# Performance work log

Hardware: AMD Instinct MI355X
Metric: run time of the kernel (lower is better)

Reference implementation:

```python
import jax, jax.numpy as jnp
import numpy as np

B, L, ENC, DEC, ATT = 128, 196, 2048, 512, 512

def setup_inputs() -> dict:
    key = jax.random.key(0)
    ks = jax.random.split(key, 8)
    s_enc = 1.0 / np.sqrt(ENC)
    s_dec = 1.0 / np.sqrt(DEC)
    s_att = 1.0 / np.sqrt(ATT)
    return {
        "encoder_out": jax.random.normal(ks[0], (B, L, ENC), jnp.float32),
        "decoder_hidden": jax.random.normal(ks[1], (B, DEC), jnp.float32),
        "We": jax.random.uniform(ks[2], (ENC, ATT), jnp.float32, -s_enc, s_enc),
        "be": jax.random.uniform(ks[3], (ATT,), jnp.float32, -s_enc, s_enc),
        "Wd": jax.random.uniform(ks[4], (DEC, ATT), jnp.float32, -s_dec, s_dec),
        "bd": jax.random.uniform(ks[5], (ATT,), jnp.float32, -s_dec, s_dec),
        "wa": jax.random.uniform(ks[6], (ATT,), jnp.float32, -s_att, s_att),
        "ba": jax.random.uniform(ks[7], (), jnp.float32, -s_att, s_att),
    }

def reference(encoder_out, decoder_hidden, We, be, Wd, bd, wa, ba):
    # encoder_out: [B, L, ENC]; decoder_hidden: [B, DEC]
    enc_map = jnp.einsum('ble,ea->bla', encoder_out, We) + be          # [B, L, A]
    dec_map = decoder_hidden @ Wd + bd                                  # [B, A]
    scores = jnp.tanh(enc_map + dec_map[:, None, :]) @ wa + ba         # [B, L]
    alphas = jax.nn.softmax(scores, axis=1)                             # [B, L]
    context = jnp.einsum('bl,ble->be', alphas, encoder_out)             # [B, ENC]
    return (context, alphas)
```

## Files before the change

kernel.cpp:

```cpp
#include <hip/hip_runtime.h>

#define B_   128
#define L_   196
#define ENC_ 2048
#define DEC_ 512
#define ATT_ 512
#define M_   (B_ * L_)

typedef _Float16 f16x8 __attribute__((ext_vector_type(8)));
typedef __fp16   h16x2 __attribute__((ext_vector_type(2)));
typedef float    f32x4 __attribute__((ext_vector_type(4)));

#define FENCE_LDS_BARRIER()                                        \
    do {                                                           \
        asm volatile("s_waitcnt lgkmcnt(0)" ::: "memory");         \
        __builtin_amdgcn_s_barrier();                              \
        __builtin_amdgcn_sched_barrier(0);                         \
    } while (0)

__device__ __forceinline__ void gload16(const _Float16* g, _Float16* l) {
    __builtin_amdgcn_global_load_lds(
        (const __attribute__((address_space(1))) void*)g,
        (__attribute__((address_space(3))) void*)l, 16, 0, 0);
}


__global__ void wets2_kernel(const float* __restrict__ We, _Float16* __restrict__ WeTs) {
    int u = blockIdx.x * 256 + threadIdx.x;
    int col = u & 255;
    int k8  = (u >> 8) & 3;
    int kt  = (u >> 10) & 63;
    int nt  = u >> 16;
    int n  = nt * 256 + col;
    int k0 = kt * 32 + k8 * 8;
    f16x8 h;
#pragma unroll
    for (int j = 0; j < 8; ++j) h[j] = (_Float16)We[(k0 + j) * ATT_ + n];
    *reinterpret_cast<f16x8*>(WeTs + (size_t)u * 8) = h;
}

__global__ void decmap_kernel(const float* __restrict__ dh, const float* __restrict__ Wd,
                              const float* __restrict__ bd, float* __restrict__ dec) {
    int b = blockIdx.x;
    int a = threadIdx.x;
    float acc = bd[a];
    const float* dhp = dh + b * DEC_;
#pragma unroll 8
    for (int k = 0; k < DEC_; ++k) acc += dhp[k] * Wd[k * ATT_ + a];
    dec[b * ATT_ + a] = acc;
}

__global__ __launch_bounds__(512, 2)
void gemm_score_kernel(const float* __restrict__ enc,
                       const _Float16* __restrict__ WeTs,
                       const float* __restrict__ be,
                       const float* __restrict__ wa,
                       const float* __restrict__ dec,
                       float* __restrict__ scores) {
    __shared__ _Float16 As[2][16384];
    __shared__ _Float16 Bs[2][16384];
    __shared__ float red[4][256];

    int bid = blockIdx.x;
    int xcd = bid & 7, kk = bid >> 3;
    int sid = (xcd < 4 ? xcd * 25 : 100 + (xcd - 4) * 24) + kk;
    int mtile = sid >> 1;
    int nt2   = sid & 1;

    int tid  = threadIdx.x;
    int lane = tid & 63, wid = tid >> 6;
    int wm = wid >> 2, wn = wid & 3;
    int l15 = lane & 15, lg = lane >> 4;

    int arow = tid >> 1;
    int h    = tid & 1;
    const float* ag = enc + (size_t)(mtile * 256 + arow) * ENC_ + h * 16;
    int wu0 = (2 * h) * 256 + (arow ^ (4 * h));
    int wu1 = (2 * h + 1) * 256 + (arow ^ (4 * h + 2));

    const _Float16* bsrc = WeTs + (size_t)nt2 * 65536 * 8;

    int aro0 = (lg * 256 + ((wm * 128 + l15) ^ (2 * lg))) * 8;
    int bfo  = (lg * 256 + wn * 64 + l15) * 8;

    f32x4 areg[8];

    f32x4 acc[8][4];
#pragma unroll
    for (int mi = 0; mi < 8; ++mi)
#pragma unroll
        for (int ni = 0; ni < 4; ++ni) acc[mi][ni] = (f32x4){0.f, 0.f, 0.f, 0.f};

    auto loadA = [&](int p) {
        const float* a = ag + p * 64;
#pragma unroll
        for (int ks = 0; ks < 2; ++ks)
#pragma unroll
            for (int j = 0; j < 4; ++j)
                areg[ks * 4 + j] = *reinterpret_cast<const f32x4*>(a + ks * 32 + j * 4);
    };
    auto writeA = [&](int buf) {
        _Float16* Ap = As[buf];
#pragma unroll
        for (int ks = 0; ks < 2; ++ks) {
            union { h16x2 h2[4]; f16x8 h8; } cv;
            cv.h2[0] = __builtin_amdgcn_cvt_pkrtz(areg[ks * 4 + 0][0], areg[ks * 4 + 0][1]);
            cv.h2[1] = __builtin_amdgcn_cvt_pkrtz(areg[ks * 4 + 0][2], areg[ks * 4 + 0][3]);
            cv.h2[2] = __builtin_amdgcn_cvt_pkrtz(areg[ks * 4 + 1][0], areg[ks * 4 + 1][1]);
            cv.h2[3] = __builtin_amdgcn_cvt_pkrtz(areg[ks * 4 + 1][2], areg[ks * 4 + 1][3]);
            *reinterpret_cast<f16x8*>(Ap + (wu0 + ks * 1024) * 8) = cv.h8;
            cv.h2[0] = __builtin_amdgcn_cvt_pkrtz(areg[ks * 4 + 2][0], areg[ks * 4 + 2][1]);
            cv.h2[1] = __builtin_amdgcn_cvt_pkrtz(areg[ks * 4 + 2][2], areg[ks * 4 + 2][3]);
            cv.h2[2] = __builtin_amdgcn_cvt_pkrtz(areg[ks * 4 + 3][0], areg[ks * 4 + 3][1]);
            cv.h2[3] = __builtin_amdgcn_cvt_pkrtz(areg[ks * 4 + 3][2], areg[ks * 4 + 3][3]);
            *reinterpret_cast<f16x8*>(Ap + (wu1 + ks * 1024) * 8) = cv.h8;
        }
    };
    auto dmab = [&](int buf, int p) {
        const _Float16* s = bsrc + (size_t)p * 2048 * 8;
#pragma unroll
        for (int j = 0; j < 4; ++j)
            gload16(s + (j * 512 + tid) * 8, &Bs[buf][(j * 512 + tid) * 8]);
    };
    auto compute = [&](int buf) {
        const _Float16* Ap = As[buf];
        const _Float16* Bp = Bs[buf];
#pragma unroll
        for (int ks = 0; ks < 2; ++ks) {
            f16x8 af[8], bf[4];
#pragma unroll
            for (int mi = 0; mi < 8; ++mi)
                af[mi] = *reinterpret_cast<const f16x8*>(Ap + ks * 8192 + aro0 + mi * 128);
#pragma unroll
            for (int ni = 0; ni < 4; ++ni)
                bf[ni] = *reinterpret_cast<const f16x8*>(Bp + ks * 8192 + bfo + ni * 128);
            __builtin_amdgcn_s_setprio(1);
#pragma unroll
            for (int mi = 0; mi < 8; ++mi)
#pragma unroll
                for (int ni = 0; ni < 4; ++ni)
                    acc[mi][ni] = __builtin_amdgcn_mfma_f32_16x16x32_f16(
                        af[mi], bf[ni], acc[mi][ni], 0, 0, 0);
            __builtin_amdgcn_s_setprio(0);
        }
    };

    loadA(0);
    dmab(0, 0);
    writeA(0);
    asm volatile("s_waitcnt vmcnt(0)" ::: "memory");
    FENCE_LDS_BARRIER();

    for (int p = 0; p < 32; ++p) {
        int pn = p + 1 < 32 ? p + 1 : 31;
        loadA(pn);
        dmab((p + 1) & 1, pn);
        __builtin_amdgcn_sched_barrier(0);
        compute(p & 1);
        __builtin_amdgcn_sched_barrier(0);
        writeA((p + 1) & 1);
        asm volatile("s_waitcnt vmcnt(0)" ::: "memory");
        FENCE_LDS_BARRIER();
    }

    float rsum[8][4];
#pragma unroll
    for (int mi = 0; mi < 8; ++mi)
#pragma unroll
        for (int j = 0; j < 4; ++j) rsum[mi][j] = 0.f;

    int rb = mtile * 256 + wm * 128;
#pragma unroll
    for (int ni = 0; ni < 4; ++ni) {
        int n = nt2 * 256 + wn * 64 + ni * 16 + l15;
        float wav = wa[n];
        float bev = be[n];
#pragma unroll
        for (int mi = 0; mi < 8; ++mi) {
#pragma unroll
            for (int j = 0; j < 4; ++j) {
                int row = rb + mi * 16 + lg * 4 + j;
                int b = row / L_;
                float x = acc[mi][ni][j] + bev + dec[b * ATT_ + n];
                float e = __expf(2.0f * x);
                float t = 1.0f - 2.0f / (e + 1.0f);
                rsum[mi][j] += t * wav;
            }
        }
    }
#pragma unroll
    for (int mi = 0; mi < 8; ++mi) {
#pragma unroll
        for (int j = 0; j < 4; ++j) {
            float v = rsum[mi][j];
            v += __shfl_xor(v, 1);
            v += __shfl_xor(v, 2);
            v += __shfl_xor(v, 4);
            v += __shfl_xor(v, 8);
            if (l15 == 0) red[wn][wm * 128 + mi * 16 + lg * 4 + j] = v;
        }
    }
    __syncthreads();
    if (tid < 256)
        scores[(size_t)nt2 * M_ + mtile * 256 + tid] =
            red[0][tid] + red[1][tid] + red[2][tid] + red[3][tid];
}

__global__ void softmax_kernel(const float* __restrict__ scores, float* __restrict__ alphas) {
    int b = blockIdx.x, t = threadIdx.x;
    int lane = t & 63, wid = t >> 6;
    __shared__ float red[4];
    float s = 0.f, val = -1e30f;
    if (t < L_) {
        int r = b * L_ + t;
        s = scores[r] + scores[M_ + r];
        val = s;
    }
    float m = val;
#pragma unroll
    for (int off = 1; off < 64; off <<= 1) m = fmaxf(m, __shfl_xor(m, off));
    if (lane == 0) red[wid] = m;
    __syncthreads();
    m = fmaxf(fmaxf(red[0], red[1]), fmaxf(red[2], red[3]));
    float e = (t < L_) ? __expf(s - m) : 0.f;
    float sum = e;
#pragma unroll
    for (int off = 1; off < 64; off <<= 1) sum += __shfl_xor(sum, off);
    __syncthreads();
    if (lane == 0) red[wid] = sum;
    __syncthreads();
    sum = red[0] + red[1] + red[2] + red[3];
    if (t < L_) alphas[b * L_ + t] = e / sum;
}

__global__ void context_kernel(const float* __restrict__ enc, const float* __restrict__ alphas,
                               float* __restrict__ ctx) {
    int b = blockIdx.x >> 2;
    int ec = blockIdx.x & 3;
    int e = ec * 512 + threadIdx.x * 2;
    const float* ep = enc + (size_t)b * L_ * ENC_ + e;
    const float* ap = alphas + b * L_;
    float ax = 0.f, ay = 0.f;
#pragma unroll 4
    for (int l = 0; l < L_; ++l) {
        float a = ap[l];
        float2 v = *reinterpret_cast<const float2*>(ep + (size_t)l * ENC_);
        ax += a * v.x;
        ay += a * v.y;
    }
    float2 r; r.x = ax; r.y = ay;
    *reinterpret_cast<float2*>(&ctx[b * ENC_ + e]) = r;
}

extern "C" void kernel_launch(void* const* d_in, const int* in_sizes, int n_in,
                              void* d_out, int out_size, void* d_ws, size_t ws_size,
                              hipStream_t stream) {
    const float* enc = (const float*)d_in[0];
    const float* dh  = (const float*)d_in[1];
    const float* We  = (const float*)d_in[2];
    const float* be  = (const float*)d_in[3];
    const float* Wd  = (const float*)d_in[4];
    const float* bd  = (const float*)d_in[5];
    const float* wa  = (const float*)d_in[6];

    float* out    = (float*)d_out;
    float* ctx    = out;
    float* alphas = out + B_ * ENC_;

    char* ws = (char*)d_ws;
    float*    dec     = (float*)ws;
    _Float16* WeTs2   = (_Float16*)(ws + 262144);
    float*    scores  = (float*)(ws + 2359296);

    hipLaunchKernelGGL(wets2_kernel,      dim3(512), dim3(256), 0, stream, We, WeTs2);
    hipLaunchKernelGGL(decmap_kernel,     dim3(128), dim3(512), 0, stream, dh, Wd, bd, dec);
    hipLaunchKernelGGL(gemm_score_kernel, dim3(196), dim3(512), 0, stream, enc, WeTs2, be, wa, dec, scores);
    hipLaunchKernelGGL(softmax_kernel,    dim3(128), dim3(256), 0, stream, scores, alphas);
    hipLaunchKernelGGL(context_kernel,    dim3(512), dim3(256), 0, stream, enc, alphas, ctx);
}
```

Baseline: 166.1 us.

## Use 1024-thread GEMM blocks with smaller K-steps and per-wave tiles

Switches the fused encoder-GEMM/score kernel from 512 to 1024 threads per block (16 waves). Each wave now computes a 64x64 tile instead of 128x64, and the K step drops from 64 to 32, which halves the LDS buffers and accumulator registers. The main loop is manually unrolled over double buffers, and the explicit vmcnt wait and setprio hints are removed. The aim is to hide latency with more waves, at the cost of more barriers per unit of work and less MFMA work between synchronisations.

```diff
diff --git a/kernel.cpp b/kernel.cpp
--- a/kernel.cpp
+++ b/kernel.cpp
@@ -50,15 +50,15 @@
     dec[b * ATT_ + a] = acc;
 }
 
-__global__ __launch_bounds__(512, 2)
+__global__ __launch_bounds__(1024, 4)
 void gemm_score_kernel(const float* __restrict__ enc,
                        const _Float16* __restrict__ WeTs,
                        const float* __restrict__ be,
                        const float* __restrict__ wa,
                        const float* __restrict__ dec,
                        float* __restrict__ scores) {
-    __shared__ _Float16 As[2][16384];
-    __shared__ _Float16 Bs[2][16384];
+    __shared__ _Float16 As[2][8192];
+    __shared__ _Float16 Bs[2][8192];
     __shared__ float red[4][256];
 
     int bid = blockIdx.x;
@@ -72,111 +72,99 @@
     int wm = wid >> 2, wn = wid & 3;
     int l15 = lane & 15, lg = lane >> 4;
 
-    int arow = tid >> 1;
-    int h    = tid & 1;
-    const float* ag = enc + (size_t)(mtile * 256 + arow) * ENC_ + h * 16;
-    int wu0 = (2 * h) * 256 + (arow ^ (4 * h));
-    int wu1 = (2 * h + 1) * 256 + (arow ^ (4 * h + 2));
-
-    const _Float16* bsrc = WeTs + (size_t)nt2 * 65536 * 8;
-
-    int aro0 = (lg * 256 + ((wm * 128 + l15) ^ (2 * lg))) * 8;
-    int bfo  = (lg * 256 + wn * 64 + l15) * 8;
-
-    f32x4 areg[8];
-
-    f32x4 acc[8][4];
-#pragma unroll
-    for (int mi = 0; mi < 8; ++mi)
+    int arow = tid >> 2;
+    int ac8  = tid & 3;
+    const float* ag = enc + (size_t)(mtile * 256 + arow) * ENC_ + ac8 * 8;
+    int wa0 = (ac8 * 256 + (arow ^ (2 * ac8))) * 8;
+
+    const _Float16* bsrc = WeTs + ((size_t)nt2 * 65536 + tid) * 8;
+
+    int afo = (lg * 256 + ((wm * 64 + l15) ^ (2 * lg))) * 8;
+    int axor = (l15 ^ (2 * lg)) - l15;
+    int bfo = (lg * 256 + wn * 64 + l15) * 8;
+
+    f32x4 areg[2];
+
+    f32x4 acc[4][4];
+#pragma unroll
+    for (int mi = 0; mi < 4; ++mi)
 #pragma unroll
         for (int ni = 0; ni < 4; ++ni) acc[mi][ni] = (f32x4){0.f, 0.f, 0.f, 0.f};
 
-    auto loadA = [&](int p) {
-        const float* a = ag + p * 64;
-#pragma unroll
-        for (int ks = 0; ks < 2; ++ks)
-#pragma unroll
-            for (int j = 0; j < 4; ++j)
-                areg[ks * 4 + j] = *reinterpret_cast<const f32x4*>(a + ks * 32 + j * 4);
+    auto loadA = [&](int kt) {
+        const float* a = ag + kt * 32;
+        areg[0] = *reinterpret_cast<const f32x4*>(a);
+        areg[1] = *reinterpret_cast<const f32x4*>(a + 4);
     };
     auto writeA = [&](int buf) {
-        _Float16* Ap = As[buf];
-#pragma unroll
-        for (int ks = 0; ks < 2; ++ks) {
-            union { h16x2 h2[4]; f16x8 h8; } cv;
-            cv.h2[0] = __builtin_amdgcn_cvt_pkrtz(areg[ks * 4 + 0][0], areg[ks * 4 + 0][1]);
-            cv.h2[1] = __builtin_amdgcn_cvt_pkrtz(areg[ks * 4 + 0][2], areg[ks * 4 + 0][3]);
-            cv.h2[2] = __builtin_amdgcn_cvt_pkrtz(areg[ks * 4 + 1][0], areg[ks * 4 + 1][1]);
-            cv.h2[3] = __builtin_amdgcn_cvt_pkrtz(areg[ks * 4 + 1][2], areg[ks * 4 + 1][3]);
-            *reinterpret_cast<f16x8*>(Ap + (wu0 + ks * 1024) * 8) = cv.h8;
-            cv.h2[0] = __builtin_amdgcn_cvt_pkrtz(areg[ks * 4 + 2][0], areg[ks * 4 + 2][1]);
-            cv.h2[1] = __builtin_amdgcn_cvt_pkrtz(areg[ks * 4 + 2][2], areg[ks * 4 + 2][3]);
-            cv.h2[2] = __builtin_amdgcn_cvt_pkrtz(areg[ks * 4 + 3][0], areg[ks * 4 + 3][1]);
-            cv.h2[3] = __builtin_amdgcn_cvt_pkrtz(areg[ks * 4 + 3][2], areg[ks * 4 + 3][3]);
-            *reinterpret_cast<f16x8*>(Ap + (wu1 + ks * 1024) * 8) = cv.h8;
-        }
-    };
-    auto dmab = [&](int buf, int p) {
-        const _Float16* s = bsrc + (size_t)p * 2048 * 8;
-#pragma unroll
-        for (int j = 0; j < 4; ++j)
-            gload16(s + (j * 512 + tid) * 8, &Bs[buf][(j * 512 + tid) * 8]);
+        union { h16x2 h2[4]; f16x8 h8; } cv;
+        cv.h2[0] = __builtin_amdgcn_cvt_pkrtz(areg[0][0], areg[0][1]);
+        cv.h2[1] = __builtin_amdgcn_cvt_pkrtz(areg[0][2], areg[0][3]);
+        cv.h2[2] = __builtin_amdgcn_cvt_pkrtz(areg[1][0], areg[1][1]);
+        cv.h2[3] = __builtin_amdgcn_cvt_pkrtz(areg[1][2], areg[1][3]);
+        *reinterpret_cast<f16x8*>(&As[buf][wa0]) = cv.h8;
+    };
+    auto dmab = [&](int buf, int kt) {
+        gload16(bsrc + (size_t)kt * 8192, &Bs[buf][tid * 8]);
     };
     auto compute = [&](int buf) {
         const _Float16* Ap = As[buf];
         const _Float16* Bp = Bs[buf];
-#pragma unroll
-        for (int ks = 0; ks < 2; ++ks) {
-            f16x8 af[8], bf[4];
-#pragma unroll
-            for (int mi = 0; mi < 8; ++mi)
-                af[mi] = *reinterpret_cast<const f16x8*>(Ap + ks * 8192 + aro0 + mi * 128);
+        f16x8 af[4], bf[4];
+#pragma unroll
+        for (int mi = 0; mi < 4; ++mi)
+            af[mi] = *reinterpret_cast<const f16x8*>(
+                Ap + (lg * 256 + wm * 64 + mi * 16 + l15 + axor) * 8);
+#pragma unroll
+        for (int ni = 0; ni < 4; ++ni)
+            bf[ni] = *reinterpret_cast<const f16x8*>(Bp + bfo + ni * 128);
+#pragma unroll
+        for (int mi = 0; mi < 4; ++mi)
 #pragma unroll
             for (int ni = 0; ni < 4; ++ni)
-                bf[ni] = *reinterpret_cast<const f16x8*>(Bp + ks * 8192 + bfo + ni * 128);
-            __builtin_amdgcn_s_setprio(1);
-#pragma unroll
-            for (int mi = 0; mi < 8; ++mi)
-#pragma unroll
-                for (int ni = 0; ni < 4; ++ni)
-                    acc[mi][ni] = __builtin_amdgcn_mfma_f32_16x16x32_f16(
-                        af[mi], bf[ni], acc[mi][ni], 0, 0, 0);
-            __builtin_amdgcn_s_setprio(0);
-        }
-    };
-
+                acc[mi][ni] = __builtin_amdgcn_mfma_f32_16x16x32_f16(
+                    af[mi], bf[ni], acc[mi][ni], 0, 0, 0);
+    };
+
+    dmab(0, 0);
     loadA(0);
-    dmab(0, 0);
     writeA(0);
-    asm volatile("s_waitcnt vmcnt(0)" ::: "memory");
     FENCE_LDS_BARRIER();
 
-    for (int p = 0; p < 32; ++p) {
-        int pn = p + 1 < 32 ? p + 1 : 31;
-        loadA(pn);
-        dmab((p + 1) & 1, pn);
-        __builtin_amdgcn_sched_barrier(0);
-        compute(p & 1);
-        __builtin_amdgcn_sched_barrier(0);
-        writeA((p + 1) & 1);
-        asm volatile("s_waitcnt vmcnt(0)" ::: "memory");
-        FENCE_LDS_BARRIER();
-    }
-
-    float rsum[8][4];
-#pragma unroll
-    for (int mi = 0; mi < 8; ++mi)
+    for (int k2 = 0; k2 < 32; ++k2) {
+        int k = k2 * 2;
+        {
+            int kn = k + 1;
+            dmab(1, kn);
+            loadA(kn);
+            compute(0);
+            writeA(1);
+            FENCE_LDS_BARRIER();
+        }
+        {
+            int kn = k + 2 < 64 ? k + 2 : 63;
+            dmab(0, kn);
+            loadA(kn);
+            compute(1);
+            writeA(0);
+            FENCE_LDS_BARRIER();
+        }
+    }
+
+    float rsum[4][4];
+#pragma unroll
+    for (int mi = 0; mi < 4; ++mi)
 #pragma unroll
         for (int j = 0; j < 4; ++j) rsum[mi][j] = 0.f;
 
-    int rb = mtile * 256 + wm * 128;
+    int rb = mtile * 256 + wm * 64;
 #pragma unroll
     for (int ni = 0; ni < 4; ++ni) {
         int n = nt2 * 256 + wn * 64 + ni * 16 + l15;
         float wav = wa[n];
         float bev = be[n];
 #pragma unroll
-        for (int mi = 0; mi < 8; ++mi) {
+        for (int mi = 0; mi < 4; ++mi) {
 #pragma unroll
             for (int j = 0; j < 4; ++j) {
                 int row = rb + mi * 16 + lg * 4 + j;
@@ -189,7 +177,7 @@
         }
     }
 #pragma unroll
-    for (int mi = 0; mi < 8; ++mi) {
+    for (int mi = 0; mi < 4; ++mi) {
 #pragma unroll
         for (int j = 0; j < 4; ++j) {
             float v = rsum[mi][j];
@@ -197,7 +185,7 @@
             v += __shfl_xor(v, 2);
             v += __shfl_xor(v, 4);
             v += __shfl_xor(v, 8);
-            if (l15 == 0) red[wn][wm * 128 + mi * 16 + lg * 4 + j] = v;
+            if (l15 == 0) red[wn][wm * 64 + mi * 16 + lg * 4 + j] = v;
         }
     }
     __syncthreads();
@@ -272,9 +260,9 @@
     _Float16* WeTs2   = (_Float16*)(ws + 262144);
     float*    scores  = (float*)(ws + 2359296);
 
-    hipLaunchKernelGGL(wets2_kernel,      dim3(512), dim3(256), 0, stream, We, WeTs2);
-    hipLaunchKernelGGL(decmap_kernel,     dim3(128), dim3(512), 0, stream, dh, Wd, bd, dec);
-    hipLaunchKernelGGL(gemm_score_kernel, dim3(196), dim3(512), 0, stream, enc, WeTs2, be, wa, dec, scores);
-    hipLaunchKernelGGL(softmax_kernel,    dim3(128), dim3(256), 0, stream, scores, alphas);
-    hipLaunchKernelGGL(context_kernel,    dim3(512), dim3(256), 0, stream, enc, alphas, ctx);
-}
+    hipLaunchKernelGGL(wets2_kernel,      dim3(512), dim3(256),  0, stream, We, WeTs2);
+    hipLaunchKernelGGL(decmap_kernel,     dim3(128), dim3(512),  0, stream, dh, Wd, bd, dec);
+    hipLaunchKernelGGL(gemm_score_kernel, dim3(196), dim3(1024), 0, stream, enc, WeTs2, be, wa, dec, scores);
+    hipLaunchKernelGGL(softmax_kernel,    dim3(128), dim3(256),  0, stream, scores, alphas);
+    hipLaunchKernelGGL(context_kernel,    dim3(512), dim3(256),  0, stream, enc, alphas, ctx);
+}
```

After: 149.5 us. 10.0% less time.

## Pre-convert encoder to fp16 and stream GEMM operands via 4-stage LDS DMA

Applied to the files above, without the earlier changes.

Adds a pass that converts the whole encoder tensor to fp16 in workspace. The GEMM then loads both operands straight into LDS with global_load_lds through a 4-buffer pipeline (K step 32), with swizzled layouts for A and a matching pre-swizzled We. The context kernel reads the fp16 copy as well. The aim is to remove register-staged fp32 loads and in-loop conversion and to halve the bytes read by the GEMM and context passes. In exchange it adds a full fp32 read plus fp16 write of the encoder, and the context sum now uses fp16-rounded encoder values, which lowers accuracy.

```diff
diff --git a/kernel.cpp b/kernel.cpp
--- a/kernel.cpp
+++ b/kernel.cpp
@@ -7,6 +7,7 @@
 #define ATT_ 512
 #define M_   (B_ * L_)
 
+typedef _Float16 f16x4v __attribute__((ext_vector_type(4)));
 typedef _Float16 f16x8 __attribute__((ext_vector_type(8)));
 typedef __fp16   h16x2 __attribute__((ext_vector_type(2)));
 typedef float    f32x4 __attribute__((ext_vector_type(4)));
@@ -25,14 +26,31 @@
 }
 
 
-__global__ void wets2_kernel(const float* __restrict__ We, _Float16* __restrict__ WeTs) {
+__global__ void enc16_kernel(const float* __restrict__ enc, _Float16* __restrict__ enc16) {
+    size_t i = ((size_t)blockIdx.x * 256 + threadIdx.x) * 8;
+    size_t stride = (size_t)gridDim.x * 256 * 8;
+    size_t total = (size_t)M_ * ENC_;
+    for (; i < total; i += stride) {
+        float4 a = *reinterpret_cast<const float4*>(enc + i);
+        float4 b = *reinterpret_cast<const float4*>(enc + i + 4);
+        union { h16x2 h2[4]; f16x8 h8; } cv;
+        cv.h2[0] = __builtin_amdgcn_cvt_pkrtz(a.x, a.y);
+        cv.h2[1] = __builtin_amdgcn_cvt_pkrtz(a.z, a.w);
+        cv.h2[2] = __builtin_amdgcn_cvt_pkrtz(b.x, b.y);
+        cv.h2[3] = __builtin_amdgcn_cvt_pkrtz(b.z, b.w);
+        *reinterpret_cast<f16x8*>(enc16 + i) = cv.h8;
+    }
+}
+
+__global__ void wets2s_kernel(const float* __restrict__ We, _Float16* __restrict__ WeTs) {
     int u = blockIdx.x * 256 + threadIdx.x;
-    int col = u & 255;
+    int cs  = u & 255;
     int k8  = (u >> 8) & 3;
     int kt  = (u >> 10) & 63;
     int nt  = u >> 16;
-    int n  = nt * 256 + col;
-    int k0 = kt * 32 + k8 * 8;
+    int col = cs ^ (2 * k8);
+    int n   = nt * 256 + col;
+    int k0  = kt * 32 + k8 * 8;
     f16x8 h;
 #pragma unroll
     for (int j = 0; j < 8; ++j) h[j] = (_Float16)We[(k0 + j) * ATT_ + n];
@@ -51,14 +69,14 @@
 }
 
 __global__ __launch_bounds__(512, 2)
-void gemm_score_kernel(const float* __restrict__ enc,
-                       const _Float16* __restrict__ WeTs,
-                       const float* __restrict__ be,
-                       const float* __restrict__ wa,
-                       const float* __restrict__ dec,
-                       float* __restrict__ scores) {
-    __shared__ _Float16 As[2][16384];
-    __shared__ _Float16 Bs[2][16384];
+void gemm16_kernel(const _Float16* __restrict__ enc16,
+                   const _Float16* __restrict__ WeTs,
+                   const float* __restrict__ be,
+                   const float* __restrict__ wa,
+                   const float* __restrict__ dec,
+                   float* __restrict__ partial) {
+    __shared__ _Float16 Ah[4][8192];
+    __shared__ _Float16 Bh[4][8192];
     __shared__ float red[4][256];
 
     int bid = blockIdx.x;
@@ -72,18 +90,18 @@
     int wm = wid >> 2, wn = wid & 3;
     int l15 = lane & 15, lg = lane >> 4;
 
-    int arow = tid >> 1;
-    int h    = tid & 1;
-    const float* ag = enc + (size_t)(mtile * 256 + arow) * ENC_ + h * 16;
-    int wu0 = (2 * h) * 256 + (arow ^ (4 * h));
-    int wu1 = (2 * h + 1) * 256 + (arow ^ (4 * h + 2));
-
-    const _Float16* bsrc = WeTs + (size_t)nt2 * 65536 * 8;
-
-    int aro0 = (lg * 256 + ((wm * 128 + l15) ^ (2 * lg))) * 8;
-    int bfo  = (lg * 256 + wn * 64 + l15) * 8;
-
-    f32x4 areg[8];
+    int rs  = tid & 255;
+    int ks1 = tid >> 8;
+    int ks2 = ks1 + 2;
+    int row1 = rs ^ (2 * ks1);
+    int row2 = rs ^ (2 * ks2);
+    const _Float16* srcA1 = enc16 + (size_t)(mtile * 256 + row1) * ENC_ + ks1 * 8;
+    const _Float16* srcA2 = enc16 + (size_t)(mtile * 256 + row2) * ENC_ + ks2 * 8;
+
+    const _Float16* srcB = WeTs + ((size_t)nt2 * 65536 + tid) * 8;
+
+    int aoff = (lg * 256 + wm * 128 + (l15 ^ (2 * lg))) * 8;
+    int boff = (lg * 256 + wn * 64 + (l15 ^ (2 * lg))) * 8;
 
     f32x4 acc[8][4];
 #pragma unroll
@@ -91,77 +109,77 @@
 #pragma unroll
         for (int ni = 0; ni < 4; ++ni) acc[mi][ni] = (f32x4){0.f, 0.f, 0.f, 0.f};
 
-    auto loadA = [&](int p) {
-        const float* a = ag + p * 64;
-#pragma unroll
-        for (int ks = 0; ks < 2; ++ks)
-#pragma unroll
-            for (int j = 0; j < 4; ++j)
-                areg[ks * 4 + j] = *reinterpret_cast<const f32x4*>(a + ks * 32 + j * 4);
-    };
-    auto writeA = [&](int buf) {
-        _Float16* Ap = As[buf];
-#pragma unroll
-        for (int ks = 0; ks < 2; ++ks) {
-            union { h16x2 h2[4]; f16x8 h8; } cv;
-            cv.h2[0] = __builtin_amdgcn_cvt_pkrtz(areg[ks * 4 + 0][0], areg[ks * 4 + 0][1]);
-            cv.h2[1] = __builtin_amdgcn_cvt_pkrtz(areg[ks * 4 + 0][2], areg[ks * 4 + 0][3]);
-            cv.h2[2] = __builtin_amdgcn_cvt_pkrtz(areg[ks * 4 + 1][0], areg[ks * 4 + 1][1]);
-            cv.h2[3] = __builtin_amdgcn_cvt_pkrtz(areg[ks * 4 + 1][2], areg[ks * 4 + 1][3]);
-            *reinterpret_cast<f16x8*>(Ap + (wu0 + ks * 1024) * 8) = cv.h8;
-            cv.h2[0] = __builtin_amdgcn_cvt_pkrtz(areg[ks * 4 + 2][0], areg[ks * 4 + 2][1]);
-            cv.h2[1] = __builtin_amdgcn_cvt_pkrtz(areg[ks * 4 + 2][2], areg[ks * 4 + 2][3]);
-            cv.h2[2] = __builtin_amdgcn_cvt_pkrtz(areg[ks * 4 + 3][0], areg[ks * 4 + 3][1]);
-            cv.h2[3] = __builtin_amdgcn_cvt_pkrtz(areg[ks * 4 + 3][2], areg[ks * 4 + 3][3]);
-            *reinterpret_cast<f16x8*>(Ap + (wu1 + ks * 1024) * 8) = cv.h8;
-        }
-    };
-    auto dmab = [&](int buf, int p) {
-        const _Float16* s = bsrc + (size_t)p * 2048 * 8;
-#pragma unroll
-        for (int j = 0; j < 4; ++j)
-            gload16(s + (j * 512 + tid) * 8, &Bs[buf][(j * 512 + tid) * 8]);
-    };
-    auto compute = [&](int buf) {
-        const _Float16* Ap = As[buf];
-        const _Float16* Bp = Bs[buf];
-#pragma unroll
-        for (int ks = 0; ks < 2; ++ks) {
-            f16x8 af[8], bf[4];
-#pragma unroll
-            for (int mi = 0; mi < 8; ++mi)
-                af[mi] = *reinterpret_cast<const f16x8*>(Ap + ks * 8192 + aro0 + mi * 128);
-#pragma unroll
-            for (int ni = 0; ni < 4; ++ni)
-                bf[ni] = *reinterpret_cast<const f16x8*>(Bp + ks * 8192 + bfo + ni * 128);
-            __builtin_amdgcn_s_setprio(1);
-#pragma unroll
-            for (int mi = 0; mi < 8; ++mi)
-#pragma unroll
-                for (int ni = 0; ni < 4; ++ni)
-                    acc[mi][ni] = __builtin_amdgcn_mfma_f32_16x16x32_f16(
-                        af[mi], bf[ni], acc[mi][ni], 0, 0, 0);
-            __builtin_amdgcn_s_setprio(0);
-        }
-    };
-
-    loadA(0);
-    dmab(0, 0);
-    writeA(0);
+#define DMAH(BUF, H)                                                     \
+    do {                                                                 \
+        gload16(srcA1 + (H) * 32, &Ah[BUF][tid * 8]);                    \
+        gload16(srcA2 + (H) * 32, &Ah[BUF][tid * 8 + 4096]);             \
+        gload16(srcB + (size_t)(H) * 8192,        &Bh[BUF][tid * 8]);    \
+        gload16(srcB + (size_t)(H) * 8192 + 4096, &Bh[BUF][tid * 8 + 4096]); \
+    } while (0)
+
+#define COMPUTE(BUF)                                                     \
+    do {                                                                 \
+        f16x8 af[8], bf[4];                                              \
+        _Pragma("unroll")                                                \
+        for (int mi = 0; mi < 8; ++mi)                                   \
+            af[mi] = *reinterpret_cast<const f16x8*>(&Ah[BUF][aoff + mi * 128]); \
+        _Pragma("unroll")                                                \
+        for (int ni = 0; ni < 4; ++ni)                                   \
+            bf[ni] = *reinterpret_cast<const f16x8*>(&Bh[BUF][boff + ni * 128]); \
+        asm volatile("s_waitcnt lgkmcnt(0)" ::: "memory");               \
+        __builtin_amdgcn_sched_barrier(0);                               \
+        __builtin_amdgcn_s_setprio(1);                                   \
+        _Pragma("unroll")                                                \
+        for (int mi = 0; mi < 8; ++mi)                                   \
+            _Pragma("unroll")                                            \
+            for (int ni = 0; ni < 4; ++ni)                               \
+                acc[mi][ni] = __builtin_amdgcn_mfma_f32_16x16x32_f16(    \
+                    af[mi], bf[ni], acc[mi][ni], 0, 0, 0);               \
+        __builtin_amdgcn_s_setprio(0);                                   \
+    } while (0)
+
+#define PHASE(H, BUF, DBUF)                                              \
+    do {                                                                 \
+        DMAH(DBUF, (H) + 3);                                             \
+        __builtin_amdgcn_sched_barrier(0);                               \
+        COMPUTE(BUF);                                                    \
+        asm volatile("s_waitcnt vmcnt(8)" ::: "memory");                 \
+        __builtin_amdgcn_sched_barrier(0);                               \
+        FENCE_LDS_BARRIER();                                             \
+    } while (0)
+
+    DMAH(0, 0);
+    DMAH(1, 1);
+    DMAH(2, 2);
+    asm volatile("s_waitcnt vmcnt(8)" ::: "memory");
+    __builtin_amdgcn_sched_barrier(0);
+    FENCE_LDS_BARRIER();
+
+    for (int h4 = 0; h4 < 15; ++h4) {
+        int h = h4 * 4;
+        PHASE(h + 0, 0, 3);
+        PHASE(h + 1, 1, 0);
+        PHASE(h + 2, 2, 1);
+        PHASE(h + 3, 3, 2);
+    }
+    DMAH(3, 63);
+    __builtin_amdgcn_sched_barrier(0);
+    COMPUTE(0);
+    asm volatile("s_waitcnt vmcnt(8)" ::: "memory");
+    __builtin_amdgcn_sched_barrier(0);
+    FENCE_LDS_BARRIER();
+    COMPUTE(1);
+    asm volatile("s_waitcnt vmcnt(4)" ::: "memory");
+    __builtin_amdgcn_sched_barrier(0);
+    FENCE_LDS_BARRIER();
+    COMPUTE(2);
     asm volatile("s_waitcnt vmcnt(0)" ::: "memory");
+    __builtin_amdgcn_sched_barrier(0);
     FENCE_LDS_BARRIER();
-
-    for (int p = 0; p < 32; ++p) {
-        int pn = p + 1 < 32 ? p + 1 : 31;
-        loadA(pn);
-        dmab((p + 1) & 1, pn);
-        __builtin_amdgcn_sched_barrier(0);
-        compute(p & 1);
-        __builtin_amdgcn_sched_barrier(0);
-        writeA((p + 1) & 1);
-        asm volatile("s_waitcnt vmcnt(0)" ::: "memory");
-        FENCE_LDS_BARRIER();
-    }
+    COMPUTE(3);
+#undef PHASE
+#undef COMPUTE
+#undef DMAH
 
     float rsum[8][4];
 #pragma unroll
@@ -202,18 +220,18 @@
     }
     __syncthreads();
     if (tid < 256)
-        scores[(size_t)nt2 * M_ + mtile * 256 + tid] =
+        partial[(size_t)nt2 * M_ + mtile * 256 + tid] =
             red[0][tid] + red[1][tid] + red[2][tid] + red[3][tid];
 }
 
-__global__ void softmax_kernel(const float* __restrict__ scores, float* __restrict__ alphas) {
+__global__ void softmax_kernel(const float* __restrict__ partial, float* __restrict__ alphas) {
     int b = blockIdx.x, t = threadIdx.x;
     int lane = t & 63, wid = t >> 6;
     __shared__ float red[4];
     float s = 0.f, val = -1e30f;
     if (t < L_) {
         int r = b * L_ + t;
-        s = scores[r] + scores[M_ + r];
+        s = partial[r] + partial[M_ + r];
         val = s;
     }
     float m = val;
@@ -233,23 +251,26 @@
     if (t < L_) alphas[b * L_ + t] = e / sum;
 }
 
-__global__ void context_kernel(const float* __restrict__ enc, const float* __restrict__ alphas,
-                               float* __restrict__ ctx) {
-    int b = blockIdx.x >> 2;
-    int ec = blockIdx.x & 3;
-    int e = ec * 512 + threadIdx.x * 2;
-    const float* ep = enc + (size_t)b * L_ * ENC_ + e;
+__global__ void context16_kernel(const _Float16* __restrict__ enc16,
+                                 const float* __restrict__ alphas,
+                                 float* __restrict__ ctx) {
+    int b = blockIdx.x >> 1;
+    int ec = blockIdx.x & 1;
+    int e = ec * 1024 + threadIdx.x * 4;
+    const _Float16* ep = enc16 + (size_t)b * L_ * ENC_ + e;
     const float* ap = alphas + b * L_;
-    float ax = 0.f, ay = 0.f;
+    float a0 = 0.f, a1 = 0.f, a2 = 0.f, a3 = 0.f;
 #pragma unroll 4
     for (int l = 0; l < L_; ++l) {
         float a = ap[l];
-        float2 v = *reinterpret_cast<const float2*>(ep + (size_t)l * ENC_);
-        ax += a * v.x;
-        ay += a * v.y;
-    }
-    float2 r; r.x = ax; r.y = ay;
-    *reinterpret_cast<float2*>(&ctx[b * ENC_ + e]) = r;
+        f16x4v v = *reinterpret_cast<const f16x4v*>(ep + (size_t)l * ENC_);
+        a0 += a * (float)v[0];
+        a1 += a * (float)v[1];
+        a2 += a * (float)v[2];
+        a3 += a * (float)v[3];
+    }
+    float4 r; r.x = a0; r.y = a1; r.z = a2; r.w = a3;
+    *reinterpret_cast<float4*>(&ctx[b * ENC_ + e]) = r;
 }
 
 extern "C" void kernel_launch(void* const* d_in, const int* in_sizes, int n_in,
@@ -269,12 +290,15 @@
 
     char* ws = (char*)d_ws;
     float*    dec     = (float*)ws;
-    _Float16* WeTs2   = (_Float16*)(ws + 262144);
-    float*    scores  = (float*)(ws + 2359296);
-
-    hipLaunchKernelGGL(wets2_kernel,      dim3(512), dim3(256), 0, stream, We, WeTs2);
-    hipLaunchKernelGGL(decmap_kernel,     dim3(128), dim3(512), 0, stream, dh, Wd, bd, dec);
-    hipLaunchKernelGGL(gemm_score_kernel, dim3(196), dim3(512), 0, stream, enc, WeTs2, be, wa, dec, scores);
-    hipLaunchKernelGGL(softmax_kernel,    dim3(128), dim3(256), 0, stream, scores, alphas);
-    hipLaunchKernelGGL(context_kernel,    dim3(512), dim3(256), 0, stream, enc, alphas, ctx);
-}
+    _Float16* WeTs2s  = (_Float16*)(ws + 262144);
+    float*    partial = (float*)(ws + 2359296);
+    _Float16* enc16   = (_Float16*)(ws + 4194304);
+
+    hipLaunchKernelGGL(enc16_kernel,     dim3(4096), dim3(256), 0, stream, enc, enc16);
+    hipLaunchKernelGGL(wets2s_kernel,    dim3(512),  dim3(256), 0, stream, We, WeTs2s);
+    hipLaunchKernelGGL(decmap_kernel,    dim3(128),  dim3(512), 0, stream, dh, Wd, bd, dec);
+    hipLaunchKernelGGL(gemm16_kernel,    dim3(196),  dim3(512), 0, stream,
+                       enc16, WeTs2s, be, wa, dec, partial);
+    hipLaunchKernelGGL(softmax_kernel,   dim3(128),  dim3(256), 0, stream, partial, alphas);
+    hipLaunchKernelGGL(context16_kernel, dim3(256),  dim3(256), 0, stream, enc16, alphas, ctx);
+}
```

New measurement: 206.1 us. 24.1% more time.
